# Kernel optimization log

Measured on AMD Instinct MI355X. Metric: run time of the kernel, lower is better.

The kernel has to match this reference:

```python
import jax, jax.numpy as jnp
import numpy as np

BUCKET = 32   # bucket_size hard-coded in module
HEADS = 8
LN_EPS = 1e-5
SELF_ATTN_VALUE = -5e4  # TOKEN_SELF_ATTN_VALUE from reformer-pytorch


def _layer_norm(x, g, b):
    m = jnp.mean(x, axis=-1, keepdims=True)
    v = jnp.mean((x - m) ** 2, axis=-1, keepdims=True)
    return (x - m) / jnp.sqrt(v + LN_EPS) * g + b


def _lsh_attention(qk, v, rot):
    # qk, v: (B=b*h, T, Dh); rot: (Dh, n_buckets//2); n_hashes = 1
    B, T, D = qk.shape
    n_buckets = T // BUCKET
    # hash: random rotations, argmax over [r, -r]
    r = jnp.einsum('btf,fi->bti', qk, rot)                 # (B, T, n_buckets//2)
    r = jnp.concatenate([r, -r], axis=-1)                  # (B, T, n_buckets)
    buckets = jnp.argmax(r, axis=-1)                       # (B, T) int
    t = jnp.arange(T)
    key = buckets * T + t                                  # unique sort key
    sticker = jnp.argsort(key, axis=-1)                    # (B, T) permutation
    undo = jnp.argsort(sticker, axis=-1)
    sqk = jnp.take_along_axis(qk, sticker[..., None], axis=1)
    sv = jnp.take_along_axis(v, sticker[..., None], axis=1)
    # chunk into n_buckets chunks of size BUCKET
    bq_t = sticker.reshape(B, n_buckets, BUCKET)
    bq = sqk.reshape(B, n_buckets, BUCKET, D)
    bv = sv.reshape(B, n_buckets, BUCKET, D)
    nrm = jnp.sqrt(jnp.sum(bq * bq, axis=-1, keepdims=True))
    bk = bq / jnp.maximum(nrm, 1e-12)                      # shared-QK: keys are unit-norm queries
    def look_one_back(xx):
        return jnp.concatenate([xx, jnp.roll(xx, 1, axis=1)], axis=2)
    bk = look_one_back(bk)
    bvv = look_one_back(bv)
    bkv_t = look_one_back(bq_t)
    dots = jnp.einsum('bcie,bcje->bcij', bq, bk) * (D ** -0.5)  # (B, C, 32, 64)
    self_mask = bq_t[:, :, :, None] == bkv_t[:, :, None, :]
    dots = jnp.where(self_mask, SELF_ATTN_VALUE, dots)
    attn = jax.nn.softmax(dots, axis=-1)
    bo = jnp.einsum('bcij,bcje->bcie', attn, bvv)
    so = bo.reshape(B, T, D)
    return jnp.take_along_axis(so, undo[..., None], axis=1)   # unsort (n_hashes=1 -> probs=1)


def _lsh_self_attention(h, w_qk, w_v, w_out, b_out, rot):
    b, t, d = h.shape
    dh = d // HEADS
    qk = (h @ w_qk).reshape(b, t, HEADS, dh).transpose(0, 2, 1, 3).reshape(b * HEADS, t, dh)
    vv = (h @ w_v).reshape(b, t, HEADS, dh).transpose(0, 2, 1, 3).reshape(b * HEADS, t, dh)
    o = _lsh_attention(qk, vv, rot)
    o = o.reshape(b, HEADS, t, dh).transpose(0, 2, 1, 3).reshape(b, t, d)
    return o @ w_out + b_out


def setup_inputs() -> dict:
    key = jax.random.key(0)
    ks = jax.random.split(key, 8)
    B, T, D, F = 8, 4096, 512, 2048
    dh, nb = D // HEADS, T // BUCKET
    s = 0.02
    return {
        'x': jax.random.normal(ks[0], (B, T, D), jnp.float32),
        'w_qk': jax.random.normal(ks[1], (D, D), jnp.float32) * s,
        'w_v': jax.random.normal(ks[2], (D, D), jnp.float32) * s,
        'w_out': jax.random.normal(ks[3], (D, D), jnp.float32) * s,
        'b_out': jnp.zeros((D,), jnp.float32),
        'ln1_g': jnp.ones((D,), jnp.float32),
        'ln1_b': jnp.zeros((D,), jnp.float32),
        'w_ff1': jax.random.normal(ks[4], (D, F), jnp.float32) * s,
        'b_ff1': jnp.zeros((F,), jnp.float32),
        'w_ff2': jax.random.normal(ks[5], (F, D), jnp.float32) * s,
        'b_ff2': jnp.zeros((D,), jnp.float32),
        'ln2_g': jnp.ones((D,), jnp.float32),
        'ln2_b': jnp.zeros((D,), jnp.float32),
        'rotations': jax.random.normal(ks[6], (dh, nb // 2), jnp.float32),
    }


def reference(x, w_qk, w_v, w_out, b_out, ln1_g, ln1_b, w_ff1, b_ff1,
              w_ff2, b_ff2, ln2_g, ln2_b, rotations):
    # y1 = x + Attn(LN1(x)); y2 = x + FFN(LN2(y1)); out = mean(y1, y2)
    h1 = _layer_norm(x, ln1_g, ln1_b)
    y1 = x + _lsh_self_attention(h1, w_qk, w_v, w_out, b_out, rotations)
    h2 = _layer_norm(y1, ln2_g, ln2_b)
    ffn = jax.nn.relu(h2 @ w_ff1 + b_ff1) @ w_ff2 + b_ff2
    y2 = x + ffn
    return 0.5 * (y1 + y2)
```

## Files before the change

kernel.cpp:

```cpp
#include <hip/hip_runtime.h>
#include <stdint.h>

typedef _Float16 f16;
typedef _Float16 f16x8 __attribute__((ext_vector_type(8)));
typedef float    f32x4 __attribute__((ext_vector_type(4)));
typedef unsigned long long u64;

__device__ __forceinline__ void gload16(const void* g, void* l) {
  __builtin_amdgcn_global_load_lds(
      (__attribute__((address_space(1))) void*)g,
      (__attribute__((address_space(3))) void*)l, 16, 0, 0);
}

#define MFMA_QUAD(q, af) \
  _Pragma("unroll") for (int m2 = 0; m2 < 2; ++m2) \
  _Pragma("unroll") for (int nt = 0; nt < 4; ++nt) \
  _Pragma("unroll") for (int kk = 0; kk < 2; ++kk) \
    acc[(q)*2 + m2][nt] = __builtin_amdgcn_mfma_f32_16x16x32_f16( \
        af[m2][kk], bf[nt][kk], acc[(q)*2 + m2][nt], 0, 0, 0);

#define RD_A(dst, abase, q2) \
  _Pragma("unroll") for (int m2 = 0; m2 < 2; ++m2) \
  _Pragma("unroll") for (int kk = 0; kk < 2; ++kk) { \
    const int lr = (q2)*32 + m2*16 + l15; \
    dst[m2][kk] = *(const f16x8*)&abase[lr*64 + (((kk*4 + l4) ^ (lr & 7)) << 3)]; }

#define RD_B(bbase) \
  _Pragma("unroll") for (int nt = 0; nt < 4; ++nt) \
  _Pragma("unroll") for (int kk = 0; kk < 2; ++kk) { \
    const int lr = brow + nt*16 + l15; \
    bf[nt][kk] = *(const f16x8*)&bbase[lr*64 + (((kk*4 + l4) ^ (lr & 7)) << 3)]; }

#define PH_PRE() \
  __builtin_amdgcn_s_barrier(); \
  asm volatile("s_waitcnt lgkmcnt(0)" ::: "memory"); \
  __builtin_amdgcn_sched_barrier(0); \
  __builtin_amdgcn_s_setprio(1);

#define PH_POST() \
  __builtin_amdgcn_s_setprio(0); \
  __builtin_amdgcn_s_barrier(); \
  __builtin_amdgcn_sched_barrier(0);

template<int EPI>
__global__ __launch_bounds__(512, 2)
void gemm256(const f16* __restrict__ A, int lda,
             const f16* __restrict__ Bt, int ldb,
             int K, int N,
             float* __restrict__ outf, f16* __restrict__ outh,
             f16* __restrict__ outh2,
             const float* __restrict__ bias,
             const float* __restrict__ add1)
{
  __shared__ __align__(16) f16 lds[65536];
  const int tid = threadIdx.x, lane = tid & 63;
  const int wid = tid >> 6;
  const int wm = wid >> 2, wn = wid & 3;
  const int l15 = lane & 15, l4 = lane >> 4;

  const int gx = gridDim.x;
  int lid = blockIdx.y * gx + blockIdx.x;
  const int cpx = (gx * gridDim.y) >> 3;
  lid = (lid & 7) * cpx + (lid >> 3);
  const long bm0 = (long)(lid / gx) * 256;
  const long bn0 = (long)(lid % gx) * 256;

  const int rs = tid >> 3, cs = tid & 7;
  const int cg = cs ^ (rs & 7);
  const int nkt = K >> 6;
  const int nmask = nkt - 1;

  auto stageA = [&](int d, int half, int kt) {
    f16* dst = &lds[(d * 4 + half) * 8192];
    const long kb = (long)kt * 64 + cg * 8;
    const f16* src = A + (bm0 + half * 128) * lda + kb;
#pragma unroll
    for (int rr = 0; rr < 2; ++rr) {
      const int row = rs + rr * 64;
      gload16(src + (long)row * lda, dst + row * 64 + cs * 8);
    }
  };
  auto stageB = [&](int d, int half, int kt) {
    f16* dst = &lds[(d * 4 + 2 + half) * 8192];
    const long kb = (long)kt * 64 + cg * 8;
    const f16* src = Bt + (bn0 + half * 128) * ldb + kb;
#pragma unroll
    for (int rr = 0; rr < 2; ++rr) {
      const int row = rs + rr * 64;
      gload16(src + (long)row * ldb, dst + row * 64 + cs * 8);
    }
  };

  const f16* aBase0 = &lds[(0 + wm) * 8192];
  const f16* aBase1 = &lds[(4 + wm) * 8192];
  const f16* bBase0 = &lds[(2 + (wn >> 1)) * 8192];
  const f16* bBase1 = &lds[(6 + (wn >> 1)) * 8192];
  const int brow = (wn & 1) * 64;

  f32x4 acc[8][4];
#pragma unroll
  for (int i = 0; i < 8; ++i)
#pragma unroll
    for (int j = 0; j < 4; ++j) acc[i][j] = f32x4{0.f, 0.f, 0.f, 0.f};
  f16x8 bf[4][2], afA[2][2], afB[2][2];

  stageB(0, 0, 0); stageB(0, 1, 0); stageA(0, 0, 0); stageA(0, 1, 0);
  asm volatile("s_waitcnt vmcnt(4)" ::: "memory");
  stageB(1, 0, 1); stageB(1, 1, 1); stageA(1, 0, 1);
  asm volatile("s_waitcnt vmcnt(6)" ::: "memory");
  __builtin_amdgcn_s_barrier();
  __builtin_amdgcn_sched_barrier(0);

  for (int j = 0; j < nkt; j += 2) {
    const int t2 = (j + 2) & nmask, t3 = (j + 3) & nmask;
    RD_B(bBase0); RD_A(afA, aBase0, 0);
    stageA(1, 1, (j + 1) & nmask);
    asm volatile("s_waitcnt lgkmcnt(8)" ::: "memory");
    PH_PRE(); MFMA_QUAD(0, afA); PH_POST();
    RD_A(afB, aBase0, 1); RD_A(afA, aBase0, 2);
    stageB(0, 0, t2);
    PH_PRE(); MFMA_QUAD(1, afB); PH_POST();
    RD_A(afB, aBase0, 3);
    stageB(0, 1, t2);
    PH_PRE(); MFMA_QUAD(2, afA); PH_POST();
    stageA(0, 0, t2);
    asm volatile("s_waitcnt vmcnt(6)" ::: "memory");
    PH_PRE(); MFMA_QUAD(3, afB); PH_POST();
    RD_B(bBase1); RD_A(afA, aBase1, 0);
    stageA(0, 1, t2);
    asm volatile("s_waitcnt lgkmcnt(8)" ::: "memory");
    PH_PRE(); MFMA_QUAD(0, afA); PH_POST();
    RD_A(afB, aBase1, 1); RD_A(afA, aBase1, 2);
    stageB(1, 0, t3);
    PH_PRE(); MFMA_QUAD(1, afB); PH_POST();
    RD_A(afB, aBase1, 3);
    stageB(1, 1, t3);
    PH_PRE(); MFMA_QUAD(2, afA); PH_POST();
    stageA(1, 0, t3);
    asm volatile("s_waitcnt vmcnt(6)" ::: "memory");
    PH_PRE(); MFMA_QUAD(3, afB); PH_POST();
  }
  asm volatile("s_waitcnt vmcnt(0)" ::: "memory");

#pragma unroll
  for (int mt = 0; mt < 8; ++mt)
#pragma unroll
    for (int nt = 0; nt < 4; ++nt)
#pragma unroll
      for (int r = 0; r < 4; ++r) {
        const long grow = bm0 + wm * 128 + mt * 16 + l4 * 4 + r;
        const long gcol = bn0 + wn * 64 + nt * 16 + l15;
        const float c = acc[mt][nt][r];
        if constexpr (EPI == 12) {
          const long idx = grow * (long)N + gcol;
          outf[idx] = c + bias[gcol] + add1[idx];
        } else if constexpr (EPI == 13) {
          const long idx = grow * (long)N + gcol;
          outh[idx] = (f16)fmaxf(c + bias[gcol], 0.f);
        } else if constexpr (EPI == 17) {
          const int bb = (int)(grow >> 12), tt = (int)(grow & 4095);
          const int hcol = (int)(bn0 >> 6) + wn;
          const int is_v = hcol >> 3, h = hcol & 7;
          f16* base = is_v ? outh2 : outh;
          base[(((long)bb * 8 + h) * 4096 + tt) * 64 + nt * 16 + l15] = (f16)c;
        }
      }
}

#define RD2_B(bbase) \
  _Pragma("unroll") for (int nt = 0; nt < 4; ++nt) \
  _Pragma("unroll") for (int kk = 0; kk < 2; ++kk) { \
    const int lr = brow + nt*16 + l15; \
    bf[nt][kk] = *(const f16x8*)&bbase[lr*64 + (((kk*4 + l4) ^ (lr & 7)) << 3)]; }

#define RD2_A(dst, abase, mt) \
  _Pragma("unroll") for (int kk = 0; kk < 2; ++kk) { \
    const int lr = arow + (mt)*16 + l15; \
    dst[kk] = *(const f16x8*)&abase[lr*64 + (((kk*4 + l4) ^ (lr & 7)) << 3)]; }

#define MFMA_Q1(mt, af) \
  _Pragma("unroll") for (int nt = 0; nt < 4; ++nt) \
  _Pragma("unroll") for (int kk = 0; kk < 2; ++kk) \
    acc[mt][nt] = __builtin_amdgcn_mfma_f32_16x16x32_f16( \
        af[kk], bf[nt][kk], acc[mt][nt], 0, 0, 0);

__global__ __launch_bounds__(512, 2)
void ffn2_8ph(const f16* __restrict__ A, const f16* __restrict__ Bt,
              const f16* __restrict__ sxyh, const float* __restrict__ bias,
              float* __restrict__ outf)
{
  __shared__ __align__(16) f16 lds[49152];
  const int tid = threadIdx.x, lane = tid & 63;
  const int wid = tid >> 6;
  const int wm = wid >> 1, wn = wid & 1;
  const int l15 = lane & 15, l4 = lane >> 4;

  const int gx = gridDim.x;
  int lid = blockIdx.y * gx + blockIdx.x;
  const int cpx = (gx * gridDim.y) >> 3;
  lid = (lid & 7) * cpx + (lid >> 3);
  const long bm0 = (long)(lid / gx) * 256;
  const long bn0 = (long)(lid % gx) * 128;

  const int rs = tid >> 3, cs = tid & 7;
  const int cg = cs ^ (rs & 7);
  const int nmask = 31;

  auto stageA = [&](int d, int half, int kt) {
    f16* dst = &lds[(d * 3 + half) * 8192];
    const long kb = (long)kt * 64 + cg * 8;
    const f16* src = A + (bm0 + half * 128) * 2048 + kb;
#pragma unroll
    for (int rr = 0; rr < 2; ++rr) {
      const int row = rs + rr * 64;
      gload16(src + (long)row * 2048, dst + row * 64 + cs * 8);
    }
  };
  auto stageB = [&](int d, int kt) {
    f16* dst = &lds[(d * 3 + 2) * 8192];
    const long kb = (long)kt * 64 + cg * 8;
    const f16* src = Bt + bn0 * 2048 + kb;
#pragma unroll
    for (int rr = 0; rr < 2; ++rr) {
      const int row = rs + rr * 64;
      gload16(src + (long)row * 2048, dst + row * 64 + cs * 8);
    }
  };

  const f16* aBase0 = &lds[(0 + (wm >> 1)) * 8192];
  const f16* aBase1 = &lds[(3 + (wm >> 1)) * 8192];
  const f16* bBase0 = &lds[2 * 8192];
  const f16* bBase1 = &lds[5 * 8192];
  const int arow = (wm & 1) * 64;
  const int brow = wn * 64;

  f32x4 acc[4][4];
#pragma unroll
  for (int i = 0; i < 4; ++i)
#pragma unroll
    for (int j = 0; j < 4; ++j) acc[i][j] = f32x4{0.f, 0.f, 0.f, 0.f};
  f16x8 bf[4][2], afA[2], afB[2];

  stageB(0, 0); stageA(0, 0, 0); stageA(0, 1, 0);
  stageB(1, 1); stageA(1, 0, 1); stageA(1, 1, 1);
  asm volatile("s_waitcnt vmcnt(6)" ::: "memory");
  __builtin_amdgcn_s_barrier();
  __builtin_amdgcn_sched_barrier(0);

  for (int j = 0; j < 32; j += 2) {
    const int t2 = (j + 2) & nmask, t3 = (j + 3) & nmask;
    RD2_B(bBase0); RD2_A(afA, aBase0, 0);
    asm volatile("s_waitcnt lgkmcnt(8)" ::: "memory");
    PH_PRE(); MFMA_Q1(0, afA); PH_POST();
    RD2_A(afB, aBase0, 1); RD2_A(afA, aBase0, 2);
    stageB(0, t2);
    PH_PRE(); MFMA_Q1(1, afB); PH_POST();
    RD2_A(afB, aBase0, 3);
    PH_PRE(); MFMA_Q1(2, afA); PH_POST();
    stageA(0, 0, t2); stageA(0, 1, t2);
    asm volatile("s_waitcnt vmcnt(6)" ::: "memory");
    PH_PRE(); MFMA_Q1(3, afB); PH_POST();
    RD2_B(bBase1); RD2_A(afA, aBase1, 0);
    asm volatile("s_waitcnt lgkmcnt(8)" ::: "memory");
    PH_PRE(); MFMA_Q1(0, afA); PH_POST();
    RD2_A(afB, aBase1, 1); RD2_A(afA, aBase1, 2);
    stageB(1, t3);
    PH_PRE(); MFMA_Q1(1, afB); PH_POST();
    RD2_A(afB, aBase1, 3);
    PH_PRE(); MFMA_Q1(2, afA); PH_POST();
    stageA(1, 0, t3); stageA(1, 1, t3);
    asm volatile("s_waitcnt vmcnt(6)" ::: "memory");
    PH_PRE(); MFMA_Q1(3, afB); PH_POST();
  }
  asm volatile("s_waitcnt vmcnt(0)" ::: "memory");

#pragma unroll
  for (int mt = 0; mt < 4; ++mt)
#pragma unroll
    for (int nt = 0; nt < 4; ++nt)
#pragma unroll
      for (int r = 0; r < 4; ++r) {
        const long grow = bm0 + wm * 64 + mt * 16 + l4 * 4 + r;
        const long gcol = bn0 + wn * 64 + nt * 16 + l15;
        const long idx = grow * 512 + gcol;
        outf[idx] = (float)sxyh[idx] + 0.5f * (acc[mt][nt][r] + bias[gcol]);
      }
}

__global__ __launch_bounds__(256)
void ln_kernel(const float* __restrict__ in, const float* __restrict__ gam,
               const float* __restrict__ bet, f16* __restrict__ out,
               int ldo, int split, const float* __restrict__ xin,
               f16* __restrict__ sxy)
{
  const long row = (long)blockIdx.x * 4 + (threadIdx.x >> 6);
  const int lane = threadIdx.x & 63;
  const float4* p = (const float4*)(in + row * 512);
  const float4 a = p[lane * 2], b = p[lane * 2 + 1];
  float xv[8] = {a.x, a.y, a.z, a.w, b.x, b.y, b.z, b.w};
  float s = 0.f;
#pragma unroll
  for (int i = 0; i < 8; ++i) s += xv[i];
#pragma unroll
  for (int m = 32; m; m >>= 1) s += __shfl_xor(s, m);
  const float mean = s * (1.f / 512.f);
  float vs = 0.f;
#pragma unroll
  for (int i = 0; i < 8; ++i) { const float d = xv[i] - mean; vs += d * d; }
#pragma unroll
  for (int m = 32; m; m >>= 1) vs += __shfl_xor(vs, m);
  const float rstd = 1.f / sqrtf(vs * (1.f / 512.f) + 1e-5f);
  const float4* gp = (const float4*)gam;
  const float4* bp = (const float4*)bet;
  const float4 g0 = gp[lane * 2], g1 = gp[lane * 2 + 1];
  const float4 b0 = bp[lane * 2], b1 = bp[lane * 2 + 1];
  const float gg[8] = {g0.x, g0.y, g0.z, g0.w, g1.x, g1.y, g1.z, g1.w};
  const float bb[8] = {b0.x, b0.y, b0.z, b0.w, b1.x, b1.y, b1.z, b1.w};
  f16x8 vh, vl;
#pragma unroll
  for (int i = 0; i < 8; ++i) {
    const float y = (xv[i] - mean) * rstd * gg[i] + bb[i];
    const f16 hi = (f16)y;
    vh[i] = hi;
    vl[i] = (f16)((y - (float)hi) * 64.f);
  }
  f16* o = out + row * ldo + lane * 8;
  *(f16x8*)o = vh;
  if (split) *(f16x8*)(o + 512) = vl;
  if (sxy) {
    const float4* xp = (const float4*)(xin + row * 512);
    const float4 x0 = xp[lane * 2], x1 = xp[lane * 2 + 1];
    const float xx[8] = {x0.x, x0.y, x0.z, x0.w, x1.x, x1.y, x1.z, x1.w};
    f16x8 vsx;
#pragma unroll
    for (int i = 0; i < 8; ++i) vsx[i] = (f16)(0.5f * (xv[i] + xx[i]));
    *(f16x8*)(sxy + row * 512 + lane * 8) = vsx;
  }
}

__global__ __launch_bounds__(256)
void transpose_f16(const float* __restrict__ src, f16* __restrict__ dst, int K, int N)
{
  __shared__ float tile[32][33];
  const int tx = threadIdx.x & 31, ty = threadIdx.x >> 5;
  const long k0 = (long)blockIdx.y * 32, n0 = (long)blockIdx.x * 32;
#pragma unroll
  for (int i = 0; i < 4; ++i)
    tile[ty + i * 8][tx] = src[(k0 + ty + i * 8) * N + n0 + tx];
  __syncthreads();
#pragma unroll
  for (int i = 0; i < 4; ++i)
    dst[(n0 + ty + i * 8) * K + k0 + tx] = (f16)tile[tx][ty + i * 8];
}

__global__ __launch_bounds__(256)
void whash_f32(const float* __restrict__ wqk, const float* __restrict__ rot,
               float* __restrict__ WrT, f16* __restrict__ rotTh)
{
  if (blockIdx.x == 0 && blockIdx.y == 0) {
    for (int idx = threadIdx.x; idx < 4096; idx += 256) {
      const int d = idx >> 6, i = idx & 63;
      rotTh[i * 64 + d] = (f16)rot[idx];
    }
  }
  const int kk = blockIdx.x;
  const int n  = blockIdx.y * 256 + threadIdx.x;
  const int h = n >> 6, i = n & 63;
  float s = 0.f;
  for (int d = 0; d < 64; ++d)
    s += wqk[kk * 512 + h * 64 + d] * rot[d * 64 + i];
  WrT[(long)n * 512 + kk] = s;
}

__global__ __launch_bounds__(256)
void rhash4_kernel(const f16* __restrict__ gqk, const f16* __restrict__ rotTh,
                   int* __restrict__ buckets)
{
  const int tid = threadIdx.x, lane = tid & 63, w = tid >> 6;
  const int bh = blockIdx.x >> 5, tb = blockIdx.x & 31;
  const int t0 = tb * 128;
  const int l15 = lane & 15, l4 = lane >> 4;

  f16x8 br[2][4];
#pragma unroll
  for (int kk = 0; kk < 2; ++kk)
#pragma unroll
    for (int nt = 0; nt < 4; ++nt)
      br[kk][nt] = *(const f16x8*)&rotTh[(nt * 16 + l15) * 64 + kk * 32 + l4 * 8];

  const f16* gqb = gqk + ((long)bh * 4096 + t0) * 64;
  f16x8 aq[2][2];
#pragma unroll
  for (int kk = 0; kk < 2; ++kk)
#pragma unroll
    for (int mt = 0; mt < 2; ++mt)
      aq[kk][mt] = *(const f16x8*)&gqb[(long)(w * 32 + mt * 16 + l15) * 64 + kk * 32 + l4 * 8];

  f32x4 acc[2][4];
#pragma unroll
  for (int i = 0; i < 2; ++i)
#pragma unroll
    for (int j = 0; j < 4; ++j) acc[i][j] = f32x4{0.f, 0.f, 0.f, 0.f};
#pragma unroll
  for (int kk = 0; kk < 2; ++kk)
#pragma unroll
    for (int mt = 0; mt < 2; ++mt)
#pragma unroll
      for (int nt = 0; nt < 4; ++nt)
        acc[mt][nt] = __builtin_amdgcn_mfma_f32_16x16x32_f16(aq[kk][mt], br[kk][nt], acc[mt][nt], 0, 0, 0);

#pragma unroll
  for (int mt = 0; mt < 2; ++mt)
#pragma unroll
    for (int r = 0; r < 4; ++r) {
      const float v0 = acc[mt][0][r], v1 = acc[mt][1][r];
      const float v2 = acc[mt][2][r], v3 = acc[mt][3][r];
      unsigned int k0 = (__float_as_uint(fabsf(v0)) & ~63u) | (unsigned int)(63 - l15);
      unsigned int k1 = (__float_as_uint(fabsf(v1)) & ~63u) | (unsigned int)(47 - l15);
      unsigned int k2 = (__float_as_uint(fabsf(v2)) & ~63u) | (unsigned int)(31 - l15);
      unsigned int k3 = (__float_as_uint(fabsf(v3)) & ~63u) | (unsigned int)(15 - l15);
      float ss = v0 * v0 + v1 * v1 + v2 * v2 + v3 * v3;
#pragma unroll
      for (int m = 1; m < 16; m <<= 1) ss += __shfl_xor(ss, m);

      unsigned int mk = max(max(k0, k1), max(k2, k3));
#pragma unroll
      for (int m = 1; m < 16; m <<= 1) mk = max(mk, (unsigned int)__shfl_xor((int)mk, m));
      const unsigned int key1 = mk;
      const int col1 = 63 - (int)(key1 & 63u);
      const float m1f = __uint_as_float(key1 & ~63u);
      const int nt1 = col1 >> 4;
      const float vsel = (nt1 == 0) ? v0 : (nt1 == 1) ? v1 : (nt1 == 2) ? v2 : v3;
      const bool owner = (col1 & 15) == l15;
      const u64 bal = __ballot(owner && (vsel < 0.f));
      const int neg = (int)((bal >> (l4 * 16 + (col1 & 15))) & 1ull);
      const int bucket = col1 + (neg << 6);
      if (owner) {
        if (nt1 == 0) k0 = 0; else if (nt1 == 1) k1 = 0;
        else if (nt1 == 2) k2 = 0; else k3 = 0;
      }
      mk = max(max(k0, k1), max(k2, k3));
#pragma unroll
      for (int m = 1; m < 16; m <<= 1) mk = max(mk, (unsigned int)__shfl_xor((int)mk, m));
      const int col2 = 63 - (int)(mk & 63u);
      const float m2f = __uint_as_float(mk & ~63u);
      {
        const int nt2 = col2 >> 4;
        if ((col2 & 15) == l15) {
          if (nt2 == 0) k0 = 0; else if (nt2 == 1) k1 = 0;
          else if (nt2 == 2) k2 = 0; else k3 = 0;
        }
      }
      mk = max(max(k0, k1), max(k2, k3));
#pragma unroll
      for (int m = 1; m < 16; m <<= 1) mk = max(mk, (unsigned int)__shfl_xor((int)mk, m));
      const int col3 = 63 - (int)(mk & 63u);

      if (l15 == 0) {
        const int row = w * 32 + mt * 16 + l4 * 4 + r;
        const int bht = bh * 4096 + t0 + row;
        const float margin = m1f - m2f;
        const float rms = sqrtf(ss * (1.f / 64.f));
        const int flag = (margin < 0.015f * rms) ? 1 : 0;
        buckets[bht] = bucket | (col2 << 8) | (col3 << 16) | (flag << 24);
      }
    }
}

__global__ __launch_bounds__(256)
void fixup2_kernel(const f16* __restrict__ hsplit, const float* __restrict__ WrT,
                   int* __restrict__ buckets)
{
  const int wid = (blockIdx.x * 256 + threadIdx.x) >> 6;
  const int lane = threadIdx.x & 63;
  for (int batch = 0; batch < 4; ++batch) {
    const int base = wid * 256 + batch * 64;
    const int packed = buckets[base + lane];
    u64 bal = __ballot((packed >> 24) & 1);
    while (bal) {
      const int i = (int)__ffsll((long long)bal) - 1;
      bal &= bal - 1;
      const int row = base + i;
      const int pk = __shfl(packed, i);
      const int h = (row >> 12) & 7;
      const long hrow = (long)(row >> 15) * 4096 + (row & 4095);
      const f16* hp = hsplit + hrow * 1024 + lane * 8;
      const f16x8 hi = *(const f16x8*)hp;
      const f16x8 lo = *(const f16x8*)(hp + 512);
      float h1[8];
#pragma unroll
      for (int k = 0; k < 8; ++k) h1[k] = (float)hi[k] + (float)lo[k] * 0.015625f;
      const int cols[3] = { pk & 63, (pk >> 8) & 63, (pk >> 16) & 63 };
      float best = -1e30f; int bi = 999;
#pragma unroll
      for (int c = 0; c < 3; ++c) {
        const int cc = cols[c];
        const float* wp = WrT + ((long)(h * 64 + cc)) * 512 + lane * 8;
        const float4 w0 = *(const float4*)wp;
        const float4 w1 = *(const float4*)(wp + 4);
        float s = h1[0] * w0.x + h1[1] * w0.y + h1[2] * w0.z + h1[3] * w0.w
                + h1[4] * w1.x + h1[5] * w1.y + h1[6] * w1.z + h1[7] * w1.w;
#pragma unroll
        for (int m = 32; m; m >>= 1) s += __shfl_xor(s, m);
        if (s > best || (s == best && cc < bi)) { best = s; bi = cc; }
        const float ns = -s; const int ni = 64 + cc;
        if (ns > best || (ns == best && ni < bi)) { best = ns; bi = ni; }
      }
      if (lane == 0) buckets[row] = bi;
    }
  }
}

__global__ __launch_bounds__(256)
void sort_kernel(const int* __restrict__ buckets, int* __restrict__ sticker)
{
  __shared__ int bkt[4096];
  __shared__ unsigned int cnts[64][128];
  __shared__ unsigned char rnk[4096];
  __shared__ int tot[128];
  __shared__ int base[128];
  const int bh = blockIdx.x;
  const int tid = threadIdx.x;
  const int lane = tid & 63, wv = tid >> 6;

  for (int i = tid; i < 4096; i += 256) bkt[i] = buckets[(long)bh * 4096 + i] & 127;
  for (int i = tid; i < 64 * 128; i += 256) ((unsigned int*)cnts)[i] = 0u;
  __syncthreads();

  for (int it = 0; it < 16; ++it) {
    const int c = wv * 16 + it;
    const int t = c * 64 + lane;
    const int b = bkt[t];
    unsigned long long m = ~0ull;
#pragma unroll
    for (int k = 0; k < 7; ++k) {
      const bool bit = (b >> k) & 1;
      const unsigned long long bal = __ballot(bit);
      m &= bit ? bal : ~bal;
    }
    const int rk = (int)__popcll(m & ((1ull << lane) - 1ull));
    rnk[t] = (unsigned char)rk;
    if (rk == 0) cnts[c][b] = (unsigned int)__popcll(m);
  }
  __syncthreads();

  if (tid < 128) {
    unsigned int run = 0;
    for (int c = 0; c < 64; ++c) {
      const unsigned int x = cnts[c][tid];
      cnts[c][tid] = run;
      run += x;
    }
    tot[tid] = (int)run;
  }
  __syncthreads();
  if (tid == 0) {
    int run = 0;
    for (int b = 0; b < 128; ++b) { base[b] = run; run += tot[b]; }
  }
  __syncthreads();

  for (int it = 0; it < 16; ++it) {
    const int c = wv * 16 + it;
    const int t = c * 64 + lane;
    const int b = bkt[t];
    const int pos = base[b] + (int)cnts[c][b] + (int)rnk[t];
    sticker[(long)bh * 4096 + pos] = t;
  }
}

__global__ __launch_bounds__(256)
void attn2_kernel(const f16* __restrict__ gqk, const f16* __restrict__ gv,
                  const int* __restrict__ sticker, f16* __restrict__ o)
{
  __shared__ __align__(16) f16 sqk[160 * 64];
  __shared__ __align__(16) f16 sVT[64 * 168];
  __shared__ __align__(16) f16 sP[4][32 * 72];
  __shared__ float rnorm[160];
  __shared__ int st[160];

  const int tid = threadIdx.x, lane = tid & 63, w = tid >> 6;
  const int cg = blockIdx.x, bh = blockIdx.y;
  const int b = bh >> 3, h = bh & 7;
  const int p0 = cg * 128 - 32;
  const int l15 = lane & 15, l4 = lane >> 4;

  if (tid < 160) st[tid] = sticker[(long)bh * 4096 + ((p0 + tid) & 4095)] & 4095;
  __syncthreads();

  const f16* gqb = gqk + (long)bh * 4096 * 64;
#pragma unroll
  for (int it = 0; it < 5; ++it) {
    const int idx = it * 256 + tid;
    const int row = idx >> 3, ch = idx & 7;
    const int gsrc = ch ^ (row & 7);
    gload16(gqb + (long)st[row] * 64 + gsrc * 8, &sqk[idx * 8]);
  }

  const f16* gvb = gv + (long)bh * 4096 * 64;
  f16x8 va[5];
#pragma unroll
  for (int i = 0; i < 5; ++i) {
    const int row = w * 40 + i * 8 + (lane >> 3);
    va[i] = *(const f16x8*)&gvb[(long)st[row] * 64 + (lane & 7) * 8];
  }
#pragma unroll
  for (int i = 0; i < 5; ++i) {
    const int row = w * 40 + i * 8 + (lane >> 3);
    const int d0 = (lane & 7) * 8;
#pragma unroll
    for (int e = 0; e < 8; ++e) sVT[(d0 + e) * 168 + row] = va[i][e];
  }
  __syncthreads();

  if (tid < 160) {
    float s = 0.f;
#pragma unroll
    for (int g = 0; g < 8; ++g) {
      const f16x8 v = *(const f16x8*)&sqk[tid * 64 + ((g ^ (tid & 7)) << 3)];
#pragma unroll
      for (int e = 0; e < 8; ++e) { const float f = (float)v[e]; s += f * f; }
    }
    rnorm[tid] = 1.f / fmaxf(sqrtf(s), 1e-12f);
  }
  __syncthreads();

  f32x4 acc[2][4];
#pragma unroll
  for (int i = 0; i < 2; ++i)
#pragma unroll
    for (int j = 0; j < 4; ++j) acc[i][j] = f32x4{0.f, 0.f, 0.f, 0.f};

#pragma unroll
  for (int kk = 0; kk < 2; ++kk) {
    f16x8 aq[2], bk[4];
#pragma unroll
    for (int mt = 0; mt < 2; ++mt) {
      const int row = 32 + w * 32 + mt * 16 + l15;
      const int g = kk * 4 + l4;
      aq[mt] = *(const f16x8*)&sqk[row * 64 + ((g ^ (row & 7)) << 3)];
    }
#pragma unroll
    for (int nt = 0; nt < 4; ++nt) {
      const int row = w * 32 + nt * 16 + l15;
      const int g = kk * 4 + l4;
      bk[nt] = *(const f16x8*)&sqk[row * 64 + ((g ^ (row & 7)) << 3)];
    }
#pragma unroll
    for (int mt = 0; mt < 2; ++mt)
#pragma unroll
      for (int nt = 0; nt < 4; ++nt)
        acc[mt][nt] = __builtin_amdgcn_mfma_f32_16x16x32_f16(aq[mt], bk[nt], acc[mt][nt], 0, 0, 0);
  }

  float rn[4];
#pragma unroll
  for (int nt = 0; nt < 4; ++nt) rn[nt] = rnorm[w * 32 + nt * 16 + l15];

  float pinv[2][4];
#pragma unroll
  for (int mt = 0; mt < 2; ++mt)
#pragma unroll
    for (int r = 0; r < 4; ++r) {
      const int row_i = mt * 16 + l4 * 4 + r;
      float mx = -1e30f;
#pragma unroll
      for (int nt = 0; nt < 4; ++nt) {
        float v = acc[mt][nt][r] * 0.125f * rn[nt];
        if (nt * 16 + l15 == row_i + 32) v = -5e4f;
        acc[mt][nt][r] = v;
        mx = fmaxf(mx, v);
      }
#pragma unroll
      for (int m = 8; m; m >>= 1) mx = fmaxf(mx, __shfl_xor(mx, m));
      float ssum = 0.f;
#pragma unroll
      for (int nt = 0; nt < 4; ++nt) {
        const float pe = expf(acc[mt][nt][r] - mx);
        ssum += pe;
        sP[w][row_i * 72 + nt * 16 + l15] = (f16)pe;
      }
#pragma unroll
      for (int m = 8; m; m >>= 1) ssum += __shfl_xor(ssum, m);
      pinv[mt][r] = 1.f / ssum;
    }
  __syncthreads();

  f32x4 pacc[2][4];
#pragma unroll
  for (int i = 0; i < 2; ++i)
#pragma unroll
    for (int j = 0; j < 4; ++j) pacc[i][j] = f32x4{0.f, 0.f, 0.f, 0.f};

#pragma unroll
  for (int kk = 0; kk < 2; ++kk) {
    f16x8 ap[2], bv[4];
#pragma unroll
    for (int mt = 0; mt < 2; ++mt)
      ap[mt] = *(const f16x8*)&sP[w][(mt * 16 + l15) * 72 + kk * 32 + l4 * 8];
#pragma unroll
    for (int nt = 0; nt < 4; ++nt)
      bv[nt] = *(const f16x8*)&sVT[(nt * 16 + l15) * 168 + w * 32 + kk * 32 + l4 * 8];
#pragma unroll
    for (int mt = 0; mt < 2; ++mt)
#pragma unroll
      for (int nt = 0; nt < 4; ++nt)
        pacc[mt][nt] = __builtin_amdgcn_mfma_f32_16x16x32_f16(ap[mt], bv[nt], pacc[mt][nt], 0, 0, 0);
  }

  const long ob = (long)b * 4096 * 512 + h * 64;
#pragma unroll
  for (int mt = 0; mt < 2; ++mt)
#pragma unroll
    for (int r = 0; r < 4; ++r) {
      const int row_i = mt * 16 + l4 * 4 + r;
      const long t = st[32 + w * 32 + row_i];
      const float sc = pinv[mt][r];
#pragma unroll
      for (int nt = 0; nt < 4; ++nt)
        o[ob + t * 512 + nt * 16 + l15] = (f16)(pacc[mt][nt][r] * sc);
    }
}

extern "C" void kernel_launch(void* const* d_in, const int* in_sizes, int n_in,
                              void* d_out, int out_size, void* d_ws, size_t ws_size,
                              hipStream_t stream)
{
  const float* x     = (const float*)d_in[0];
  const float* w_qk  = (const float*)d_in[1];
  const float* w_v   = (const float*)d_in[2];
  const float* w_out = (const float*)d_in[3];
  const float* b_out = (const float*)d_in[4];
  const float* ln1g  = (const float*)d_in[5];
  const float* ln1b  = (const float*)d_in[6];
  const float* w_ff1 = (const float*)d_in[7];
  const float* b_ff1 = (const float*)d_in[8];
  const float* w_ff2 = (const float*)d_in[9];
  const float* b_ff2 = (const float*)d_in[10];
  const float* ln2g  = (const float*)d_in[11];
  const float* ln2b  = (const float*)d_in[12];
  const float* rot   = (const float*)d_in[13];
  float* out = (float*)d_out;

  char* ws = (char*)d_ws;
  f16* hsplit = (f16*)ws;
  f16* o_buf  = (f16*)ws;
  f16* sxy    = (f16*)ws;
  f16* h2     = (f16*)(ws + 33554432);
  f16* gqk    = (f16*)(ws + 67108864);
  f16* gv     = (f16*)(ws + 100663296);
  f16* abuf   = (f16*)(ws + 67108864);
  char* W0 = ws + 134217728;
  f16* wqkvT = (f16*)W0;
  f16* woutT = (f16*)(W0 + 1048576);
  f16* wff1T = (f16*)(W0 + 1572864);
  f16* wff2T = (f16*)(W0 + 3670016);
  float* WrT = (float*)(W0 + 5767168);
  int* buckets = (int*)(W0 + 6815744);
  int* sticker = (int*)(W0 + 7864320);
  f16* rotTh   = (f16*)(W0 + 8912896);

  const dim3 b256(256);
  const dim3 b512(512);
  transpose_f16<<<dim3(16, 16), b256, 0, stream>>>(w_qk,  wqkvT,             512, 512);
  transpose_f16<<<dim3(16, 16), b256, 0, stream>>>(w_v,   wqkvT + 512 * 512, 512, 512);
  transpose_f16<<<dim3(16, 16), b256, 0, stream>>>(w_out, woutT,             512, 512);
  transpose_f16<<<dim3(64, 16), b256, 0, stream>>>(w_ff1, wff1T,             512, 2048);
  transpose_f16<<<dim3(16, 64), b256, 0, stream>>>(w_ff2, wff2T,             2048, 512);
  whash_f32<<<dim3(512, 2), b256, 0, stream>>>(w_qk, rot, WrT, rotTh);
  ln_kernel<<<dim3(8192), b256, 0, stream>>>(x, ln1g, ln1b, hsplit, 1024, 1, nullptr, nullptr);
  gemm256<17><<<dim3(4, 128), b512, 0, stream>>>(hsplit, 1024, wqkvT, 512, 512, 1024,
      nullptr, gqk, gv, nullptr, nullptr);
  rhash4_kernel<<<dim3(2048), b256, 0, stream>>>(gqk, rotTh, buckets);
  fixup2_kernel<<<dim3(256), b256, 0, stream>>>(hsplit, WrT, buckets);
  sort_kernel<<<dim3(64), b256, 0, stream>>>(buckets, sticker);
  attn2_kernel<<<dim3(32, 64), b256, 0, stream>>>(gqk, gv, sticker, o_buf);
  gemm256<12><<<dim3(2, 128), b512, 0, stream>>>(o_buf, 512, woutT, 512, 512, 512,
      out, nullptr, nullptr, b_out, x);
  ln_kernel<<<dim3(8192), b256, 0, stream>>>(out, ln2g, ln2b, h2, 512, 0, x, sxy);
  for (int c = 0; c < 2; ++c) {
    const long roff = (long)c * 16384;
    gemm256<13><<<dim3(8, 64), b512, 0, stream>>>(h2 + roff * 512, 512, wff1T, 512,
        512, 2048, nullptr, abuf, nullptr, b_ff1, nullptr);
    ffn2_8ph<<<dim3(4, 64), b512, 0, stream>>>(abuf, wff2T, sxy + roff * 512,
        b_ff2, out + roff * 512);
  }
}
```

Before: 459.4 us.

## Replace FFN GEMMs with generic 128x128-tile, 256-thread kernel

Both FFN GEMMs now run on a new templated gemm128 kernel with 128x128 tiles, 4 waves, and a double-buffered LDS pipeline, in place of the 256x256 gemm256 (FFN1) and 256x128 ffn2_8ph (FFN2) kernels. The goal is more blocks, better occupancy and better load balance across CUs for these shapes. The cost is less data reuse per tile, so each block does more global and LDS traffic per FLOP.

```diff
diff --git a/kernel.cpp b/kernel.cpp
--- a/kernel.cpp
+++ b/kernel.cpp
@@ -11,6 +11,17 @@
       (__attribute__((address_space(1))) void*)g,
       (__attribute__((address_space(3))) void*)l, 16, 0, 0);
 }
+
+#define PH_PRE() \
+  __builtin_amdgcn_s_barrier(); \
+  asm volatile("s_waitcnt lgkmcnt(0)" ::: "memory"); \
+  __builtin_amdgcn_sched_barrier(0); \
+  __builtin_amdgcn_s_setprio(1);
+
+#define PH_POST() \
+  __builtin_amdgcn_s_setprio(0); \
+  __builtin_amdgcn_s_barrier(); \
+  __builtin_amdgcn_sched_barrier(0);
 
 #define MFMA_QUAD(q, af) \
   _Pragma("unroll") for (int m2 = 0; m2 < 2; ++m2) \
@@ -30,17 +41,6 @@
   _Pragma("unroll") for (int kk = 0; kk < 2; ++kk) { \
     const int lr = brow + nt*16 + l15; \
     bf[nt][kk] = *(const f16x8*)&bbase[lr*64 + (((kk*4 + l4) ^ (lr & 7)) << 3)]; }
-
-#define PH_PRE() \
-  __builtin_amdgcn_s_barrier(); \
-  asm volatile("s_waitcnt lgkmcnt(0)" ::: "memory"); \
-  __builtin_amdgcn_sched_barrier(0); \
-  __builtin_amdgcn_s_setprio(1);
-
-#define PH_POST() \
-  __builtin_amdgcn_s_setprio(0); \
-  __builtin_amdgcn_s_barrier(); \
-  __builtin_amdgcn_sched_barrier(0);
 
 template<int EPI>
 __global__ __launch_bounds__(512, 2)
@@ -154,9 +154,6 @@
         if constexpr (EPI == 12) {
           const long idx = grow * (long)N + gcol;
           outf[idx] = c + bias[gcol] + add1[idx];
-        } else if constexpr (EPI == 13) {
-          const long idx = grow * (long)N + gcol;
-          outh[idx] = (f16)fmaxf(c + bias[gcol], 0.f);
         } else if constexpr (EPI == 17) {
           const int bb = (int)(grow >> 12), tt = (int)(grow & 4095);
           const int hcol = (int)(bn0 >> 6) + wn;
@@ -167,29 +164,33 @@
       }
 }
 
-#define RD2_B(bbase) \
+#define RDK_B(bbase) \
   _Pragma("unroll") for (int nt = 0; nt < 4; ++nt) \
   _Pragma("unroll") for (int kk = 0; kk < 2; ++kk) { \
-    const int lr = brow + nt*16 + l15; \
+    const int lr = wn*64 + nt*16 + l15; \
     bf[nt][kk] = *(const f16x8*)&bbase[lr*64 + (((kk*4 + l4) ^ (lr & 7)) << 3)]; }
 
-#define RD2_A(dst, abase, mt) \
+#define RDK_A(dst, abase, mt) \
   _Pragma("unroll") for (int kk = 0; kk < 2; ++kk) { \
-    const int lr = arow + (mt)*16 + l15; \
+    const int lr = wm*64 + (mt)*16 + l15; \
     dst[kk] = *(const f16x8*)&abase[lr*64 + (((kk*4 + l4) ^ (lr & 7)) << 3)]; }
 
-#define MFMA_Q1(mt, af) \
+#define MFMA_P(mt, af) \
   _Pragma("unroll") for (int nt = 0; nt < 4; ++nt) \
   _Pragma("unroll") for (int kk = 0; kk < 2; ++kk) \
     acc[mt][nt] = __builtin_amdgcn_mfma_f32_16x16x32_f16( \
         af[kk], bf[nt][kk], acc[mt][nt], 0, 0, 0);
 
-__global__ __launch_bounds__(512, 2)
-void ffn2_8ph(const f16* __restrict__ A, const f16* __restrict__ Bt,
-              const f16* __restrict__ sxyh, const float* __restrict__ bias,
-              float* __restrict__ outf)
-{
-  __shared__ __align__(16) f16 lds[49152];
+template<int EPI>
+__global__ __launch_bounds__(256, 2)
+void gemm128(const f16* __restrict__ A, int lda,
+             const f16* __restrict__ Bt, int ldb,
+             int K, int N,
+             float* __restrict__ outf, f16* __restrict__ outh,
+             const float* __restrict__ bias,
+             const f16* __restrict__ sxyh)
+{
+  __shared__ __align__(16) f16 lds[32768];
   const int tid = threadIdx.x, lane = tid & 63;
   const int wid = tid >> 6;
   const int wm = wid >> 1, wn = wid & 1;
@@ -199,40 +200,39 @@
   int lid = blockIdx.y * gx + blockIdx.x;
   const int cpx = (gx * gridDim.y) >> 3;
   lid = (lid & 7) * cpx + (lid >> 3);
-  const long bm0 = (long)(lid / gx) * 256;
+  const long bm0 = (long)(lid / gx) * 128;
   const long bn0 = (long)(lid % gx) * 128;
 
   const int rs = tid >> 3, cs = tid & 7;
   const int cg = cs ^ (rs & 7);
-  const int nmask = 31;
-
-  auto stageA = [&](int d, int half, int kt) {
-    f16* dst = &lds[(d * 3 + half) * 8192];
+  const int nkt = K >> 6;
+  const int nmask = nkt - 1;
+
+  auto stageA = [&](int d, int kt) {
+    f16* dst = &lds[(d * 2) * 8192];
     const long kb = (long)kt * 64 + cg * 8;
-    const f16* src = A + (bm0 + half * 128) * 2048 + kb;
-#pragma unroll
-    for (int rr = 0; rr < 2; ++rr) {
-      const int row = rs + rr * 64;
-      gload16(src + (long)row * 2048, dst + row * 64 + cs * 8);
+    const f16* src = A + bm0 * lda + kb;
+#pragma unroll
+    for (int rd = 0; rd < 4; ++rd) {
+      const int row = rs + rd * 32;
+      gload16(src + (long)row * lda, dst + row * 64 + cs * 8);
     }
   };
   auto stageB = [&](int d, int kt) {
-    f16* dst = &lds[(d * 3 + 2) * 8192];
+    f16* dst = &lds[(d * 2 + 1) * 8192];
     const long kb = (long)kt * 64 + cg * 8;
-    const f16* src = Bt + bn0 * 2048 + kb;
-#pragma unroll
-    for (int rr = 0; rr < 2; ++rr) {
-      const int row = rs + rr * 64;
-      gload16(src + (long)row * 2048, dst + row * 64 + cs * 8);
+    const f16* src = Bt + bn0 * ldb + kb;
+#pragma unroll
+    for (int rd = 0; rd < 4; ++rd) {
+      const int row = rs + rd * 32;
+      gload16(src + (long)row * ldb, dst + row * 64 + cs * 8);
     }
   };
 
-  const f16* aBase0 = &lds[(0 + (wm >> 1)) * 8192];
-  const f16* aBase1 = &lds[(3 + (wm >> 1)) * 8192];
-  const f16* bBase0 = &lds[2 * 8192];
-  const f16* bBase1 = &lds[5 * 8192];
-  const int arow = (wm & 1) * 64;
-  const int brow = wn * 64;
+  const f16* aBase0 = &lds[0];
+  const f16* bBase0 = &lds[8192];
+  const f16* aBase1 = &lds[16384];
+  const f16* bBase1 = &lds[24576];
 
   f32x4 acc[4][4];
 #pragma unroll
@@ -241,36 +241,35 @@
     for (int j = 0; j < 4; ++j) acc[i][j] = f32x4{0.f, 0.f, 0.f, 0.f};
   f16x8 bf[4][2], afA[2], afB[2];
 
-  stageB(0, 0); stageA(0, 0, 0); stageA(0, 1, 0);
-  stageB(1, 1); stageA(1, 0, 1); stageA(1, 1, 1);
-  asm volatile("s_waitcnt vmcnt(6)" ::: "memory");
+  stageA(0, 0); stageB(0, 0); stageA(1, 1); stageB(1, 1);
+  asm volatile("s_waitcnt vmcnt(8)" ::: "memory");
   __builtin_amdgcn_s_barrier();
   __builtin_amdgcn_sched_barrier(0);
 
-  for (int j = 0; j < 32; j += 2) {
+  for (int j = 0; j < nkt; j += 2) {
     const int t2 = (j + 2) & nmask, t3 = (j + 3) & nmask;
-    RD2_B(bBase0); RD2_A(afA, aBase0, 0);
+    RDK_B(bBase0); RDK_A(afA, aBase0, 0);
     asm volatile("s_waitcnt lgkmcnt(8)" ::: "memory");
-    PH_PRE(); MFMA_Q1(0, afA); PH_POST();
-    RD2_A(afB, aBase0, 1); RD2_A(afA, aBase0, 2);
+    PH_PRE(); MFMA_P(0, afA); PH_POST();
+    RDK_A(afB, aBase0, 1); RDK_A(afA, aBase0, 2);
     stageB(0, t2);
-    PH_PRE(); MFMA_Q1(1, afB); PH_POST();
-    RD2_A(afB, aBase0, 3);
-    PH_PRE(); MFMA_Q1(2, afA); PH_POST();
-    stageA(0, 0, t2); stageA(0, 1, t2);
-    asm volatile("s_waitcnt vmcnt(6)" ::: "memory");
-    PH_PRE(); MFMA_Q1(3, afB); PH_POST();
-    RD2_B(bBase1); RD2_A(afA, aBase1, 0);
+    PH_PRE(); MFMA_P(1, afB); PH_POST();
+    RDK_A(afB, aBase0, 3);
+    PH_PRE(); MFMA_P(2, afA); PH_POST();
+    stageA(0, t2);
+    asm volatile("s_waitcnt vmcnt(8)" ::: "memory");
+    PH_PRE(); MFMA_P(3, afB); PH_POST();
+    RDK_B(bBase1); RDK_A(afA, aBase1, 0);
     asm volatile("s_waitcnt lgkmcnt(8)" ::: "memory");
-    PH_PRE(); MFMA_Q1(0, afA); PH_POST();
-    RD2_A(afB, aBase1, 1); RD2_A(afA, aBase1, 2);
+    PH_PRE(); MFMA_P(0, afA); PH_POST();
+    RDK_A(afB, aBase1, 1); RDK_A(afA, aBase1, 2);
     stageB(1, t3);
-    PH_PRE(); MFMA_Q1(1, afB); PH_POST();
-    RD2_A(afB, aBase1, 3);
-    PH_PRE(); MFMA_Q1(2, afA); PH_POST();
-    stageA(1, 0, t3); stageA(1, 1, t3);
-    asm volatile("s_waitcnt vmcnt(6)" ::: "memory");
-    PH_PRE(); MFMA_Q1(3, afB); PH_POST();
+    PH_PRE(); MFMA_P(1, afB); PH_POST();
+    RDK_A(afB, aBase1, 3);
+    PH_PRE(); MFMA_P(2, afA); PH_POST();
+    stageA(1, t3);
+    asm volatile("s_waitcnt vmcnt(8)" ::: "memory");
+    PH_PRE(); MFMA_P(3, afB); PH_POST();
   }
   asm volatile("s_waitcnt vmcnt(0)" ::: "memory");
 
@@ -282,8 +281,13 @@
       for (int r = 0; r < 4; ++r) {
         const long grow = bm0 + wm * 64 + mt * 16 + l4 * 4 + r;
         const long gcol = bn0 + wn * 64 + nt * 16 + l15;
-        const long idx = grow * 512 + gcol;
-        outf[idx] = (float)sxyh[idx] + 0.5f * (acc[mt][nt][r] + bias[gcol]);
+        const float c = acc[mt][nt][r];
+        if constexpr (EPI == 13) {
+          outh[grow * (long)N + gcol] = (f16)fmaxf(c + bias[gcol], 0.f);
+        } else if constexpr (EPI == 40) {
+          const long idx = grow * 512 + gcol;
+          outf[idx] = (float)sxyh[idx] + 0.5f * (c + bias[gcol]);
+        }
       }
 }
 
@@ -780,9 +784,9 @@
   ln_kernel<<<dim3(8192), b256, 0, stream>>>(out, ln2g, ln2b, h2, 512, 0, x, sxy);
   for (int c = 0; c < 2; ++c) {
     const long roff = (long)c * 16384;
-    gemm256<13><<<dim3(8, 64), b512, 0, stream>>>(h2 + roff * 512, 512, wff1T, 512,
-        512, 2048, nullptr, abuf, nullptr, b_ff1, nullptr);
-    ffn2_8ph<<<dim3(4, 64), b512, 0, stream>>>(abuf, wff2T, sxy + roff * 512,
-        b_ff2, out + roff * 512);
-  }
-}
+    gemm128<13><<<dim3(16, 128), b256, 0, stream>>>(h2 + roff * 512, 512, wff1T, 512,
+        512, 2048, nullptr, abuf, b_ff1, nullptr);
+    gemm128<40><<<dim3(4, 128), b256, 0, stream>>>(abuf, 2048, wff2T, 2048,
+        2048, 512, out + roff * 512, nullptr, b_ff2, sxy + roff * 512);
+  }
+}
```

After: 466.5 us. About the same (+1.5%).
